# Optimization experiments

Hardware: AMD Instinct MI355X
Metric: run time of the kernel (lower is better)

The kernel has to match this reference:

```python
import jax, jax.numpy as jnp
import numpy as np

N_NODES = 100000
N_EDGES = 1600000
D_IN = 64
D_OUT = 64
EDGE_DIM = 16


def setup_inputs() -> dict:
    key = jax.random.key(0)
    ks = jax.random.split(key, 6)
    x = jax.random.normal(ks[0], (N_NODES, D_IN), dtype=jnp.float32)
    edge_index = jax.random.randint(ks[1], (2, N_EDGES), 0, N_NODES, dtype=jnp.int64)
    edge_feature = jax.random.normal(ks[2], (N_EDGES, EDGE_DIM), dtype=jnp.float32)
    W_edge = jax.random.normal(ks[3], (EDGE_DIM, 1), dtype=jnp.float32) * (1.0 / np.sqrt(EDGE_DIM))
    b_edge = jnp.zeros((1,), dtype=jnp.float32)
    W_node = jax.random.normal(ks[4], (D_OUT, D_IN), dtype=jnp.float32) * (1.0 / np.sqrt(D_IN))
    b_node = jnp.zeros((D_OUT,), dtype=jnp.float32)
    return {"x": x, "edge_index": edge_index, "edge_feature": edge_feature,
            "W_edge": W_edge, "b_edge": b_edge, "W_node": W_node, "b_node": b_node}


def reference(x, edge_index, edge_feature, W_edge, b_edge, W_node, b_node):
    # per-edge gate: Linear(edge_dim -> 1) + Sigmoid  -> [E]
    gate = jax.nn.sigmoid(edge_feature @ W_edge + b_edge)[:, 0]
    # node projection: Linear(in -> out)  -> [N, D_OUT]
    xp = x @ W_node.T + b_node
    row = edge_index[0]  # destination (SparseTensor row)
    col = edge_index[1]  # source gathered
    num_nodes = x.shape[0]
    # weighted gather of source node features  -> [E, D_OUT]
    msg = gate[:, None] * xp[col]
    summed = jax.ops.segment_sum(msg, row, num_segments=num_nodes)
    cnt = jax.ops.segment_sum(jnp.ones((row.shape[0],), dtype=xp.dtype), row,
                              num_segments=num_nodes)
    # reduce='mean': divide by row nnz count; empty rows stay 0
    out = summed / jnp.maximum(cnt, 1.0)[:, None]
    return out
```

## Files before the change

### kernel.cpp

```cpp
#include <hip/hip_runtime.h>
#include <math.h>

#define NN 100000
#define NE 1600000
#define DD 64
#define ED 16
#define BROWS 96
#define NBIN 1042
#define NBIN_PAD 1056
#define BCAP 1920
#define EPB 2048
#define NBLKA ((NE + EPB - 1) / EPB)


__device__ __forceinline__ unsigned short f2bf(float f) {
    unsigned int b = __float_as_uint(f);
    unsigned int r = (b + 0x7FFFu + ((b >> 16) & 1u)) >> 16;
    return (unsigned short)r;
}

__global__ __launch_bounds__(256) void proj_kernel(
    const float* __restrict__ x, const float* __restrict__ Wn,
    const float* __restrict__ bn, unsigned short* __restrict__ xpb,
    int* __restrict__ cursor) {
    __shared__ float xs[128][66];
    __shared__ float ws[64][66];
    int tid = threadIdx.x;
    if (blockIdx.x == 0) {
        for (int i = tid; i < NBIN_PAD; i += 256) cursor[i] = i * BCAP;
    }
    int n0 = blockIdx.x * 128;
    const float4* x4 = reinterpret_cast<const float4*>(x);
    const float4* Wn4 = reinterpret_cast<const float4*>(Wn);
    long limit = (long)NN * 16;
#pragma unroll
    for (int i = 0; i < 8; ++i) {
        int idx = tid + 256 * i;
        int row = idx >> 4, kq = idx & 15;
        long gidx = (long)n0 * 16 + idx;
        float4 v = (gidx < limit) ? x4[gidx] : make_float4(0.f, 0.f, 0.f, 0.f);
        xs[row][kq * 4 + 0] = v.x; xs[row][kq * 4 + 1] = v.y;
        xs[row][kq * 4 + 2] = v.z; xs[row][kq * 4 + 3] = v.w;
    }
#pragma unroll
    for (int i = 0; i < 4; ++i) {
        int idx = tid + 256 * i;
        int row = idx >> 4, kq = idx & 15;
        float4 v = Wn4[idx];
        ws[row][kq * 4 + 0] = v.x; ws[row][kq * 4 + 1] = v.y;
        ws[row][kq * 4 + 2] = v.z; ws[row][kq * 4 + 3] = v.w;
    }
    int og = tid & 15;
    int ng = tid >> 4;
    float acc[8][4];
    float b0 = bn[og * 4 + 0], b1 = bn[og * 4 + 1];
    float b2 = bn[og * 4 + 2], b3 = bn[og * 4 + 3];
#pragma unroll
    for (int i = 0; i < 8; ++i) {
        acc[i][0] = b0; acc[i][1] = b1; acc[i][2] = b2; acc[i][3] = b3;
    }
    __syncthreads();
#pragma unroll 4
    for (int kk = 0; kk < 32; ++kk) {
        float2 wv0 = *reinterpret_cast<const float2*>(&ws[og * 4 + 0][kk * 2]);
        float2 wv1 = *reinterpret_cast<const float2*>(&ws[og * 4 + 1][kk * 2]);
        float2 wv2 = *reinterpret_cast<const float2*>(&ws[og * 4 + 2][kk * 2]);
        float2 wv3 = *reinterpret_cast<const float2*>(&ws[og * 4 + 3][kk * 2]);
#pragma unroll
        for (int i = 0; i < 8; ++i) {
            float2 xv = *reinterpret_cast<const float2*>(&xs[ng * 8 + i][kk * 2]);
            acc[i][0] += xv.x * wv0.x + xv.y * wv0.y;
            acc[i][1] += xv.x * wv1.x + xv.y * wv1.y;
            acc[i][2] += xv.x * wv2.x + xv.y * wv2.y;
            acc[i][3] += xv.x * wv3.x + xv.y * wv3.y;
        }
    }
#pragma unroll
    for (int i = 0; i < 8; ++i) {
        int n = n0 + ng * 8 + i;
        if (n < NN) {
            ushort4 o;
            o.x = f2bf(acc[i][0]); o.y = f2bf(acc[i][1]);
            o.z = f2bf(acc[i][2]); o.w = f2bf(acc[i][3]);
            *reinterpret_cast<ushort4*>(xpb + (size_t)n * DD + og * 4) = o;
        }
    }
}

__global__ __launch_bounds__(512) void binAG_kernel(
    const int* __restrict__ ei, const float* __restrict__ ef,
    const float* __restrict__ We, const float* __restrict__ be,
    int* __restrict__ cursor, int2* __restrict__ binned) {
    __shared__ int cnt[NBIN_PAD];
    __shared__ int basev[NBIN_PAD];
    int tid = threadIdx.x;
    int e0 = blockIdx.x * EPB;
    for (int i = tid; i < NBIN_PAD; i += 512) cnt[i] = 0;
    __syncthreads();
    int e_base = e0 + tid * 4;
    bool ok = e_base < NE;
    int4 r, c;
    float4 f0, f1, f2, f3, f4, f5, f6, f7, f8, f9, fa, fb, fc, fd, fe, ff;
    int s0 = 0, s1 = 0, s2 = 0, s3 = 0;
    int b0 = 0, b1 = 0, b2 = 0, b3 = 0;
    if (ok) {
        r = *reinterpret_cast<const int4*>(ei + e_base);
        c = *reinterpret_cast<const int4*>(ei + NE + e_base);
        const float4* p = reinterpret_cast<const float4*>(ef + (size_t)e_base * ED);
        f0 = p[0];  f1 = p[1];  f2 = p[2];  f3 = p[3];
        f4 = p[4];  f5 = p[5];  f6 = p[6];  f7 = p[7];
        f8 = p[8];  f9 = p[9];  fa = p[10]; fb = p[11];
        fc = p[12]; fd = p[13]; fe = p[14]; ff = p[15];
        b0 = r.x / BROWS; s0 = atomicAdd(&cnt[b0], 1);
        b1 = r.y / BROWS; s1 = atomicAdd(&cnt[b1], 1);
        b2 = r.z / BROWS; s2 = atomicAdd(&cnt[b2], 1);
        b3 = r.w / BROWS; s3 = atomicAdd(&cnt[b3], 1);
    }
    __syncthreads();
    for (int i = tid; i < NBIN_PAD; i += 512) {
        int cc = cnt[i];
        basev[i] = cc ? atomicAdd(&cursor[i], cc) : 0;
    }
    __syncthreads();
    if (ok) {
        const float4* We4 = reinterpret_cast<const float4*>(We);
        float4 w0 = We4[0], w1 = We4[1], w2 = We4[2], w3 = We4[3];
        float bb = be[0];
#define DOT(A0, A1, A2, A3) \
        (A0.x*w0.x + A0.y*w0.y + A0.z*w0.z + A0.w*w0.w + \
         A1.x*w1.x + A1.y*w1.y + A1.z*w1.z + A1.w*w1.w + \
         A2.x*w2.x + A2.y*w2.y + A2.z*w2.z + A2.w*w2.w + \
         A3.x*w3.x + A3.y*w3.y + A3.z*w3.z + A3.w*w3.w + bb)
        float g0 = 1.f / (1.f + expf(-DOT(f0, f1, f2, f3)));
        float g1 = 1.f / (1.f + expf(-DOT(f4, f5, f6, f7)));
        float g2 = 1.f / (1.f + expf(-DOT(f8, f9, fa, fb)));
        float g3 = 1.f / (1.f + expf(-DOT(fc, fd, fe, ff)));
#undef DOT
#define EMIT(BV, SV, RR, CC, GG) \
        binned[basev[BV] + SV] = \
            make_int2((((RR) - (BV) * BROWS) << 24) | (CC), __float_as_int(GG));
        EMIT(b0, s0, r.x, c.x, g0) EMIT(b1, s1, r.y, c.y, g1)
        EMIT(b2, s2, r.z, c.z, g2) EMIT(b3, s3, r.w, c.w, g3)
#undef EMIT
    }
}

__global__ __launch_bounds__(512) void binB_kernel(
    const unsigned short* __restrict__ xpb, const int* __restrict__ cursor,
    const int2* __restrict__ binned, float* __restrict__ out) {
    __shared__ int2 sorted[BCAP];
    __shared__ int hist[128];
    __shared__ int offs[128];
    __shared__ int claim[BROWS];
    int tid = threadIdx.x;
    int b = blockIdx.x;
    if (tid < 128) { hist[tid] = 0; offs[tid] = 0; }
    if (tid < BROWS) claim[tid] = 0;
    __syncthreads();
    int bstart = b * BCAP;
    int nb = cursor[b] - bstart;
    for (int t = tid; t < nb; t += 512) {
        int w = binned[bstart + t].x;
        atomicAdd(&hist[(w >> 24) & 0x7F], 1);
    }
    __syncthreads();
    if (tid < 128) offs[tid] = hist[tid];
    __syncthreads();
    for (int d = 1; d < 128; d <<= 1) {
        int add = 0;
        if (tid < 128 && tid >= d) add = offs[tid - d];
        __syncthreads();
        if (tid < 128) offs[tid] += add;
        __syncthreads();
    }
    for (int t = tid; t < nb; t += 512) {
        int2 e = binned[bstart + t];
        int rl = (e.x >> 24) & 0x7F;
        int pos = offs[rl] - hist[rl] + atomicAdd(&claim[rl], 1);
        sorted[pos] = e;
    }
    __syncthreads();
    int lane = tid & 63;
    int wv = tid >> 6;
    int q = lane >> 4;
    int ql = lane & 15;
#pragma unroll 1
    for (int i = 0; i < 12; ++i) {
        int rl = wv + 8 * i;
        int row = b * BROWS + rl;
        if (row >= NN) break;
        int dn = hist[rl];
        int s0 = offs[rl] - dn;
        float a0 = 0.f, a1 = 0.f, a2 = 0.f, a3 = 0.f;
        for (int j = 0; j < dn; j += 16) {
#pragma unroll
            for (int k = 0; k < 4; ++k) {
                int idx = j + 4 * k + q;
                int2 e = sorted[s0 + min(idx, dn - 1)];
                float g = (idx < dn) ? __int_as_float(e.y) : 0.f;
                int col = e.x & 0x1FFFF;
                uint2 u = *reinterpret_cast<const uint2*>(
                    xpb + (size_t)col * DD + ql * 4);
                a0 += g * __uint_as_float(u.x << 16);
                a1 += g * __uint_as_float(u.x & 0xFFFF0000u);
                a2 += g * __uint_as_float(u.y << 16);
                a3 += g * __uint_as_float(u.y & 0xFFFF0000u);
            }
        }
        a0 += __shfl_xor(a0, 16); a0 += __shfl_xor(a0, 32);
        a1 += __shfl_xor(a1, 16); a1 += __shfl_xor(a1, 32);
        a2 += __shfl_xor(a2, 16); a2 += __shfl_xor(a2, 32);
        a3 += __shfl_xor(a3, 16); a3 += __shfl_xor(a3, 32);
        if (q == 0) {
            float dv = fmaxf((float)dn, 1.f);
            *reinterpret_cast<float4*>(&out[(size_t)row * DD + ql * 4]) =
                make_float4(a0 / dv, a1 / dv, a2 / dv, a3 / dv);
        }
    }
}

extern "C" void kernel_launch(void* const* d_in, const int* in_sizes, int n_in,
                              void* d_out, int out_size, void* d_ws, size_t ws_size,
                              hipStream_t stream) {
    const float* x  = (const float*)d_in[0];
    const int*   ei = (const int*)d_in[1];
    const float* ef = (const float*)d_in[2];
    const float* We = (const float*)d_in[3];
    const float* be = (const float*)d_in[4];
    const float* Wn = (const float*)d_in[5];
    const float* bn = (const float*)d_in[6];
    float* out = (float*)d_out;

    unsigned short* xpb = (unsigned short*)d_ws;
    int*  cursor = (int*)d_ws + 3200000;
    int2* binned = (int2*)((int*)d_ws + 3201056);

    proj_kernel<<<(NN + 127) / 128, 256, 0, stream>>>(x, Wn, bn, xpb, cursor);
    binAG_kernel<<<NBLKA, 512, 0, stream>>>(ei, ef, We, be, cursor, binned);
    binB_kernel<<<NBIN, 512, 0, stream>>>(xpb, cursor, binned, out);
}
```

Baseline: 116.6 us.

## Double edges per thread in binning and register-cache bins in sorting pass

The binning kernel now handles 8 edges per thread (EPB 4096) and computes gates before the cursor barrier. It uses asm keep-alives to force the edge-feature loads to issue early and overlap, and adds a launch-bounds occupancy hint. The bin-sort kernel loads each bin's entries once into registers (up to 4 per thread) and reuses the histogram atomic's return value as the slot. This removes the second global read of binned and the claim atomics, at the cost of higher register pressure and half as many binning blocks.

```diff
diff --git a/kernel.cpp b/kernel.cpp
--- a/kernel.cpp
+++ b/kernel.cpp
@@ -9,9 +9,11 @@
 #define NBIN 1042
 #define NBIN_PAD 1056
 #define BCAP 1920
-#define EPB 2048
+#define EPB 4096
 #define NBLKA ((NE + EPB - 1) / EPB)
 
+
+#define KEEPF4(v) asm volatile("" :: "v"((v).x), "v"((v).y), "v"((v).z), "v"((v).w))
 
 __device__ __forceinline__ unsigned short f2bf(float f) {
     unsigned int b = __float_as_uint(f);
@@ -87,60 +89,88 @@
     }
 }
 
-__global__ __launch_bounds__(512) void binAG_kernel(
+__global__ __launch_bounds__(512, 2) void binAG_kernel(
     const int* __restrict__ ei, const float* __restrict__ ef,
     const float* __restrict__ We, const float* __restrict__ be,
     int* __restrict__ cursor, int2* __restrict__ binned) {
     __shared__ int cnt[NBIN_PAD];
     __shared__ int basev[NBIN_PAD];
     int tid = threadIdx.x;
-    int e0 = blockIdx.x * EPB;
+    long e0 = (long)blockIdx.x * EPB;
     for (int i = tid; i < NBIN_PAD; i += 512) cnt[i] = 0;
     __syncthreads();
-    int e_base = e0 + tid * 4;
-    bool ok = e_base < NE;
-    int4 r, c;
-    float4 f0, f1, f2, f3, f4, f5, f6, f7, f8, f9, fa, fb, fc, fd, fe, ff;
-    int s0 = 0, s1 = 0, s2 = 0, s3 = 0;
-    int b0 = 0, b1 = 0, b2 = 0, b3 = 0;
+    long eA = e0 + tid * 8;
+    bool ok = eA < NE;
+    int4 rA, rB, cA, cB;
+    float g0=0,g1=0,g2=0,g3=0,g4=0,g5=0,g6=0,g7=0;
+    int b0=0,b1=0,b2=0,b3=0,b4=0,b5=0,b6=0,b7=0;
+    int s0=0,s1=0,s2=0,s3=0,s4=0,s5=0,s6=0,s7=0;
+    const float4* We4 = reinterpret_cast<const float4*>(We);
+    float4 w0 = We4[0], w1 = We4[1], w2 = We4[2], w3 = We4[3];
+    float bb = be[0];
     if (ok) {
-        r = *reinterpret_cast<const int4*>(ei + e_base);
-        c = *reinterpret_cast<const int4*>(ei + NE + e_base);
-        const float4* p = reinterpret_cast<const float4*>(ef + (size_t)e_base * ED);
-        f0 = p[0];  f1 = p[1];  f2 = p[2];  f3 = p[3];
-        f4 = p[4];  f5 = p[5];  f6 = p[6];  f7 = p[7];
-        f8 = p[8];  f9 = p[9];  fa = p[10]; fb = p[11];
-        fc = p[12]; fd = p[13]; fe = p[14]; ff = p[15];
-        b0 = r.x / BROWS; s0 = atomicAdd(&cnt[b0], 1);
-        b1 = r.y / BROWS; s1 = atomicAdd(&cnt[b1], 1);
-        b2 = r.z / BROWS; s2 = atomicAdd(&cnt[b2], 1);
-        b3 = r.w / BROWS; s3 = atomicAdd(&cnt[b3], 1);
-    }
-    __syncthreads();
-    for (int i = tid; i < NBIN_PAD; i += 512) {
-        int cc = cnt[i];
-        basev[i] = cc ? atomicAdd(&cursor[i], cc) : 0;
-    }
-    __syncthreads();
-    if (ok) {
-        const float4* We4 = reinterpret_cast<const float4*>(We);
-        float4 w0 = We4[0], w1 = We4[1], w2 = We4[2], w3 = We4[3];
-        float bb = be[0];
+        rA = *reinterpret_cast<const int4*>(ei + eA);
+        rB = *reinterpret_cast<const int4*>(ei + eA + 4);
+        cA = *reinterpret_cast<const int4*>(ei + NE + eA);
+        cB = *reinterpret_cast<const int4*>(ei + NE + eA + 4);
+        const float4* p = reinterpret_cast<const float4*>(ef + eA * ED);
 #define DOT(A0, A1, A2, A3) \
         (A0.x*w0.x + A0.y*w0.y + A0.z*w0.z + A0.w*w0.w + \
          A1.x*w1.x + A1.y*w1.y + A1.z*w1.z + A1.w*w1.w + \
          A2.x*w2.x + A2.y*w2.y + A2.z*w2.z + A2.w*w2.w + \
          A3.x*w3.x + A3.y*w3.y + A3.z*w3.z + A3.w*w3.w + bb)
-        float g0 = 1.f / (1.f + expf(-DOT(f0, f1, f2, f3)));
-        float g1 = 1.f / (1.f + expf(-DOT(f4, f5, f6, f7)));
-        float g2 = 1.f / (1.f + expf(-DOT(f8, f9, fa, fb)));
-        float g3 = 1.f / (1.f + expf(-DOT(fc, fd, fe, ff)));
+        {
+            float4 f0 = p[0],  f1 = p[1],  f2 = p[2],  f3 = p[3];
+            float4 f4 = p[4],  f5 = p[5],  f6 = p[6],  f7 = p[7];
+            float4 f8 = p[8],  f9 = p[9],  fa = p[10], fb = p[11];
+            float4 fc = p[12], fd = p[13], fe = p[14], ff = p[15];
+            KEEPF4(f0); KEEPF4(f1); KEEPF4(f2); KEEPF4(f3);
+            KEEPF4(f4); KEEPF4(f5); KEEPF4(f6); KEEPF4(f7);
+            KEEPF4(f8); KEEPF4(f9); KEEPF4(fa); KEEPF4(fb);
+            KEEPF4(fc); KEEPF4(fd); KEEPF4(fe); KEEPF4(ff);
+            b0 = rA.x / BROWS; s0 = atomicAdd(&cnt[b0], 1);
+            b1 = rA.y / BROWS; s1 = atomicAdd(&cnt[b1], 1);
+            b2 = rA.z / BROWS; s2 = atomicAdd(&cnt[b2], 1);
+            b3 = rA.w / BROWS; s3 = atomicAdd(&cnt[b3], 1);
+            g0 = 1.f / (1.f + expf(-DOT(f0, f1, f2, f3)));
+            g1 = 1.f / (1.f + expf(-DOT(f4, f5, f6, f7)));
+            g2 = 1.f / (1.f + expf(-DOT(f8, f9, fa, fb)));
+            g3 = 1.f / (1.f + expf(-DOT(fc, fd, fe, ff)));
+        }
+        {
+            float4 f0 = p[16], f1 = p[17], f2 = p[18], f3 = p[19];
+            float4 f4 = p[20], f5 = p[21], f6 = p[22], f7 = p[23];
+            float4 f8 = p[24], f9 = p[25], fa = p[26], fb = p[27];
+            float4 fc = p[28], fd = p[29], fe = p[30], ff = p[31];
+            KEEPF4(f0); KEEPF4(f1); KEEPF4(f2); KEEPF4(f3);
+            KEEPF4(f4); KEEPF4(f5); KEEPF4(f6); KEEPF4(f7);
+            KEEPF4(f8); KEEPF4(f9); KEEPF4(fa); KEEPF4(fb);
+            KEEPF4(fc); KEEPF4(fd); KEEPF4(fe); KEEPF4(ff);
+            b4 = rB.x / BROWS; s4 = atomicAdd(&cnt[b4], 1);
+            b5 = rB.y / BROWS; s5 = atomicAdd(&cnt[b5], 1);
+            b6 = rB.z / BROWS; s6 = atomicAdd(&cnt[b6], 1);
+            b7 = rB.w / BROWS; s7 = atomicAdd(&cnt[b7], 1);
+            g4 = 1.f / (1.f + expf(-DOT(f0, f1, f2, f3)));
+            g5 = 1.f / (1.f + expf(-DOT(f4, f5, f6, f7)));
+            g6 = 1.f / (1.f + expf(-DOT(f8, f9, fa, fb)));
+            g7 = 1.f / (1.f + expf(-DOT(fc, fd, fe, ff)));
+        }
 #undef DOT
+    }
+    __syncthreads();
+    for (int i = tid; i < NBIN_PAD; i += 512) {
+        int cc = cnt[i];
+        basev[i] = cc ? atomicAdd(&cursor[i], cc) : 0;
+    }
+    __syncthreads();
+    if (ok) {
 #define EMIT(BV, SV, RR, CC, GG) \
         binned[basev[BV] + SV] = \
             make_int2((((RR) - (BV) * BROWS) << 24) | (CC), __float_as_int(GG));
-        EMIT(b0, s0, r.x, c.x, g0) EMIT(b1, s1, r.y, c.y, g1)
-        EMIT(b2, s2, r.z, c.z, g2) EMIT(b3, s3, r.w, c.w, g3)
+        EMIT(b0, s0, rA.x, cA.x, g0) EMIT(b1, s1, rA.y, cA.y, g1)
+        EMIT(b2, s2, rA.z, cA.z, g2) EMIT(b3, s3, rA.w, cA.w, g3)
+        EMIT(b4, s4, rB.x, cB.x, g4) EMIT(b5, s5, rB.y, cB.y, g5)
+        EMIT(b6, s6, rB.z, cB.z, g6) EMIT(b7, s7, rB.w, cB.w, g7)
 #undef EMIT
     }
 }
@@ -151,18 +181,24 @@
     __shared__ int2 sorted[BCAP];
     __shared__ int hist[128];
     __shared__ int offs[128];
-    __shared__ int claim[BROWS];
     int tid = threadIdx.x;
     int b = blockIdx.x;
-    if (tid < 128) { hist[tid] = 0; offs[tid] = 0; }
-    if (tid < BROWS) claim[tid] = 0;
+    if (tid < 128) hist[tid] = 0;
     __syncthreads();
     int bstart = b * BCAP;
     int nb = cursor[b] - bstart;
-    for (int t = tid; t < nb; t += 512) {
-        int w = binned[bstart + t].x;
-        atomicAdd(&hist[(w >> 24) & 0x7F], 1);
-    }
+    int2 e0_, e1_, e2_, e3_;
+    int r0 = 0, r1 = 0, r2 = 0, r3 = 0;
+    int s0 = -1, s1 = -1, s2 = -1, s3 = -1;
+    bool k0 = tid < nb, k1 = tid + 512 < nb, k2 = tid + 1024 < nb, k3 = tid + 1536 < nb;
+    if (k0) e0_ = binned[bstart + tid];
+    if (k1) e1_ = binned[bstart + tid + 512];
+    if (k2) e2_ = binned[bstart + tid + 1024];
+    if (k3) e3_ = binned[bstart + tid + 1536];
+    if (k0) { r0 = (e0_.x >> 24) & 0x7F; s0 = atomicAdd(&hist[r0], 1); }
+    if (k1) { r1 = (e1_.x >> 24) & 0x7F; s1 = atomicAdd(&hist[r1], 1); }
+    if (k2) { r2 = (e2_.x >> 24) & 0x7F; s2 = atomicAdd(&hist[r2], 1); }
+    if (k3) { r3 = (e3_.x >> 24) & 0x7F; s3 = atomicAdd(&hist[r3], 1); }
     __syncthreads();
     if (tid < 128) offs[tid] = hist[tid];
     __syncthreads();
@@ -173,12 +209,10 @@
         if (tid < 128) offs[tid] += add;
         __syncthreads();
     }
-    for (int t = tid; t < nb; t += 512) {
-        int2 e = binned[bstart + t];
-        int rl = (e.x >> 24) & 0x7F;
-        int pos = offs[rl] - hist[rl] + atomicAdd(&claim[rl], 1);
-        sorted[pos] = e;
-    }
+    if (s0 >= 0) sorted[offs[r0] - hist[r0] + s0] = e0_;
+    if (s1 >= 0) sorted[offs[r1] - hist[r1] + s1] = e1_;
+    if (s2 >= 0) sorted[offs[r2] - hist[r2] + s2] = e2_;
+    if (s3 >= 0) sorted[offs[r3] - hist[r3] + s3] = e3_;
     __syncthreads();
     int lane = tid & 63;
     int wv = tid >> 6;
@@ -190,13 +224,13 @@
         int row = b * BROWS + rl;
         if (row >= NN) break;
         int dn = hist[rl];
-        int s0 = offs[rl] - dn;
+        int sb = offs[rl] - dn;
         float a0 = 0.f, a1 = 0.f, a2 = 0.f, a3 = 0.f;
         for (int j = 0; j < dn; j += 16) {
 #pragma unroll
             for (int k = 0; k < 4; ++k) {
                 int idx = j + 4 * k + q;
-                int2 e = sorted[s0 + min(idx, dn - 1)];
+                int2 e = sorted[sb + min(idx, dn - 1)];
                 float g = (idx < dn) ? __int_as_float(e.y) : 0.f;
                 int col = e.x & 0x1FFFF;
                 uint2 u = *reinterpret_cast<const uint2*>(
```

Result: faster. 110.1 us (-5.5%).

## Split bin cursors into 8 groups and stage edge features via LDS DMA

Applied to the files above, without the earlier changes.

Global bin cursors are split into 8 per-group copies, chosen by block index, so scatter atomics contend less and each group writes its own sub-bin region. Edge features are loaded in chunks with global_load_lds into shared memory, with coalesced edge-index loads. The per-edge gates are computed from these chunks. The aggregation kernel gathers the 8 sub-bins into a shared staging buffer before the histogram and sort, so binned is read once from global memory. The cost is more shared memory per block, extra barriers per chunk, and a risk of overflow if a group's sub-bin exceeds its capacity of 320.

```diff
diff --git a/kernel.cpp b/kernel.cpp
--- a/kernel.cpp
+++ b/kernel.cpp
@@ -9,8 +9,12 @@
 #define NBIN 1042
 #define NBIN_PAD 1056
 #define BCAP 1920
+#define NGRP 8
+#define BCAPG 320
 #define EPB 2048
 #define NBLKA ((NE + EPB - 1) / EPB)
+
+typedef float f32x4 __attribute__((ext_vector_type(4)));
 
 
 __device__ __forceinline__ unsigned short f2bf(float f) {
@@ -27,7 +31,7 @@
     __shared__ float ws[64][66];
     int tid = threadIdx.x;
     if (blockIdx.x == 0) {
-        for (int i = tid; i < NBIN_PAD; i += 256) cursor[i] = i * BCAP;
+        for (int i = tid; i < NGRP * NBIN_PAD; i += 256) cursor[i] = i * BCAPG;
     }
     int n0 = blockIdx.x * 128;
     const float4* x4 = reinterpret_cast<const float4*>(x);
@@ -91,79 +95,97 @@
     const int* __restrict__ ei, const float* __restrict__ ef,
     const float* __restrict__ We, const float* __restrict__ be,
     int* __restrict__ cursor, int2* __restrict__ binned) {
+    __shared__ float efs[512 * 16];
     __shared__ int cnt[NBIN_PAD];
     __shared__ int basev[NBIN_PAD];
     int tid = threadIdx.x;
     int e0 = blockIdx.x * EPB;
+    int grp = blockIdx.x & (NGRP - 1);
     for (int i = tid; i < NBIN_PAD; i += 512) cnt[i] = 0;
-    __syncthreads();
-    int e_base = e0 + tid * 4;
-    bool ok = e_base < NE;
-    int4 r, c;
-    float4 f0, f1, f2, f3, f4, f5, f6, f7, f8, f9, fa, fb, fc, fd, fe, ff;
-    int s0 = 0, s1 = 0, s2 = 0, s3 = 0;
-    int b0 = 0, b1 = 0, b2 = 0, b3 = 0;
-    if (ok) {
-        r = *reinterpret_cast<const int4*>(ei + e_base);
-        c = *reinterpret_cast<const int4*>(ei + NE + e_base);
-        const float4* p = reinterpret_cast<const float4*>(ef + (size_t)e_base * ED);
-        f0 = p[0];  f1 = p[1];  f2 = p[2];  f3 = p[3];
-        f4 = p[4];  f5 = p[5];  f6 = p[6];  f7 = p[7];
-        f8 = p[8];  f9 = p[9];  fa = p[10]; fb = p[11];
-        fc = p[12]; fd = p[13]; fe = p[14]; ff = p[15];
-        b0 = r.x / BROWS; s0 = atomicAdd(&cnt[b0], 1);
-        b1 = r.y / BROWS; s1 = atomicAdd(&cnt[b1], 1);
-        b2 = r.z / BROWS; s2 = atomicAdd(&cnt[b2], 1);
-        b3 = r.w / BROWS; s3 = atomicAdd(&cnt[b3], 1);
-    }
-    __syncthreads();
+    const f32x4* We4 = reinterpret_cast<const f32x4*>(We);
+    f32x4 w0 = We4[0], w1 = We4[1], w2 = We4[2], w3 = We4[3];
+    float bb = be[0];
+    int rr[4], cc[4], bbin[4], ss[4];
+    float gg[4];
+    bool val[4];
+#pragma unroll
+    for (int c = 0; c < 4; ++c) {
+        int e = e0 + c * 512 + tid;
+        val[c] = e < NE;
+        rr[c] = val[c] ? ei[e] : 0;
+        cc[c] = val[c] ? ei[NE + e] : 0;
+        bbin[c] = 0; ss[c] = 0; gg[c] = 0.f;
+    }
+    __syncthreads();
+#pragma unroll 1
+    for (int c = 0; c < 4; ++c) {
+        int cb = e0 + c * 512;
+        if (cb < NE) {
+            const float* gsrc = ef + (size_t)cb * ED;
+#pragma unroll
+            for (int i = 0; i < 4; ++i) {
+                int u = tid + 512 * i;
+                __builtin_amdgcn_global_load_lds(
+                    (const __attribute__((address_space(1))) void*)(gsrc + (size_t)u * 4),
+                    (__attribute__((address_space(3))) void*)(efs + u * 4),
+                    16, 0, 0);
+            }
+            __syncthreads();
+            const f32x4* pe = reinterpret_cast<const f32x4*>(efs) + tid * 4;
+            f32x4 f0 = pe[0], f1 = pe[1], f2 = pe[2], f3 = pe[3];
+            float d = f0[0]*w0[0] + f0[1]*w0[1] + f0[2]*w0[2] + f0[3]*w0[3]
+                    + f1[0]*w1[0] + f1[1]*w1[1] + f1[2]*w1[2] + f1[3]*w1[3]
+                    + f2[0]*w2[0] + f2[1]*w2[1] + f2[2]*w2[2] + f2[3]*w2[3]
+                    + f3[0]*w3[0] + f3[1]*w3[1] + f3[2]*w3[2] + f3[3]*w3[3] + bb;
+            gg[c] = 1.f / (1.f + expf(-d));
+            bbin[c] = rr[c] / BROWS;
+            ss[c] = atomicAdd(&cnt[bbin[c]], 1);
+            __syncthreads();
+        }
+    }
     for (int i = tid; i < NBIN_PAD; i += 512) {
-        int cc = cnt[i];
-        basev[i] = cc ? atomicAdd(&cursor[i], cc) : 0;
-    }
-    __syncthreads();
-    if (ok) {
-        const float4* We4 = reinterpret_cast<const float4*>(We);
-        float4 w0 = We4[0], w1 = We4[1], w2 = We4[2], w3 = We4[3];
-        float bb = be[0];
-#define DOT(A0, A1, A2, A3) \
-        (A0.x*w0.x + A0.y*w0.y + A0.z*w0.z + A0.w*w0.w + \
-         A1.x*w1.x + A1.y*w1.y + A1.z*w1.z + A1.w*w1.w + \
-         A2.x*w2.x + A2.y*w2.y + A2.z*w2.z + A2.w*w2.w + \
-         A3.x*w3.x + A3.y*w3.y + A3.z*w3.z + A3.w*w3.w + bb)
-        float g0 = 1.f / (1.f + expf(-DOT(f0, f1, f2, f3)));
-        float g1 = 1.f / (1.f + expf(-DOT(f4, f5, f6, f7)));
-        float g2 = 1.f / (1.f + expf(-DOT(f8, f9, fa, fb)));
-        float g3 = 1.f / (1.f + expf(-DOT(fc, fd, fe, ff)));
-#undef DOT
-#define EMIT(BV, SV, RR, CC, GG) \
-        binned[basev[BV] + SV] = \
-            make_int2((((RR) - (BV) * BROWS) << 24) | (CC), __float_as_int(GG));
-        EMIT(b0, s0, r.x, c.x, g0) EMIT(b1, s1, r.y, c.y, g1)
-        EMIT(b2, s2, r.z, c.z, g2) EMIT(b3, s3, r.w, c.w, g3)
-#undef EMIT
+        int c2 = cnt[i];
+        basev[i] = c2 ? atomicAdd(&cursor[grp * NBIN_PAD + i], c2) : 0;
+    }
+    __syncthreads();
+#pragma unroll
+    for (int c = 0; c < 4; ++c) {
+        if (val[c]) {
+            int rl = rr[c] - bbin[c] * BROWS;
+            binned[basev[bbin[c]] + ss[c]] =
+                make_int2((rl << 24) | cc[c], __float_as_int(gg[c]));
+        }
     }
 }
 
 __global__ __launch_bounds__(512) void binB_kernel(
     const unsigned short* __restrict__ xpb, const int* __restrict__ cursor,
     const int2* __restrict__ binned, float* __restrict__ out) {
+    __shared__ int2 staged[BCAP];
     __shared__ int2 sorted[BCAP];
     __shared__ int hist[128];
     __shared__ int offs[128];
     __shared__ int claim[BROWS];
     int tid = threadIdx.x;
     int b = blockIdx.x;
-    if (tid < 128) { hist[tid] = 0; offs[tid] = 0; }
+    if (tid < 128) hist[tid] = 0;
     if (tid < BROWS) claim[tid] = 0;
     __syncthreads();
-    int bstart = b * BCAP;
-    int nb = cursor[b] - bstart;
-    for (int t = tid; t < nb; t += 512) {
-        int w = binned[bstart + t].x;
-        atomicAdd(&hist[(w >> 24) & 0x7F], 1);
-    }
-    __syncthreads();
+    int off = 0;
+#pragma unroll 1
+    for (int g = 0; g < NGRP; ++g) {
+        int cidx = g * NBIN_PAD + b;
+        int sb = cidx * BCAPG;
+        int ng = cursor[cidx] - sb;
+        for (int t = tid; t < ng; t += 512) {
+            int2 e = binned[sb + t];
+            staged[off + t] = e;
+            atomicAdd(&hist[(e.x >> 24) & 0x7F], 1);
+        }
+        off += ng;
+    }
+    __syncthreads();
+    int nb = off;
     if (tid < 128) offs[tid] = hist[tid];
     __syncthreads();
     for (int d = 1; d < 128; d <<= 1) {
@@ -174,7 +196,7 @@
         __syncthreads();
     }
     for (int t = tid; t < nb; t += 512) {
-        int2 e = binned[bstart + t];
+        int2 e = staged[t];
         int rl = (e.x >> 24) & 0x7F;
         int pos = offs[rl] - hist[rl] + atomicAdd(&claim[rl], 1);
         sorted[pos] = e;
@@ -190,13 +212,13 @@
         int row = b * BROWS + rl;
         if (row >= NN) break;
         int dn = hist[rl];
-        int s0 = offs[rl] - dn;
+        int sb2 = offs[rl] - dn;
         float a0 = 0.f, a1 = 0.f, a2 = 0.f, a3 = 0.f;
         for (int j = 0; j < dn; j += 16) {
 #pragma unroll
             for (int k = 0; k < 4; ++k) {
                 int idx = j + 4 * k + q;
-                int2 e = sorted[s0 + min(idx, dn - 1)];
+                int2 e = sorted[sb2 + min(idx, dn - 1)];
                 float g = (idx < dn) ? __int_as_float(e.y) : 0.f;
                 int col = e.x & 0x1FFFF;
                 uint2 u = *reinterpret_cast<const uint2*>(
@@ -233,7 +255,7 @@
 
     unsigned short* xpb = (unsigned short*)d_ws;
     int*  cursor = (int*)d_ws + 3200000;
-    int2* binned = (int2*)((int*)d_ws + 3201056);
+    int2* binned = (int2*)((int*)d_ws + 3208448);
 
     proj_kernel<<<(NN + 127) / 128, 256, 0, stream>>>(x, Wn, bn, xpb, cursor);
     binAG_kernel<<<NBLKA, 512, 0, stream>>>(ei, ef, We, be, cursor, binned);
```

After: 113.0 us. 1.03x faster.
